# Kernel tuning notes

Measured on AMD Instinct MI355X. Metric: run time of the kernel, lower is better.

The kernel has to match this reference:

```python
import jax, jax.numpy as jnp
import numpy as np

B, L = 64, 4096
NIN, NST = 8, 16
CIN = NIN + NST          # 24 input channels to FNO
WIDTH = 64               # hidden_channels
MODES = 32               # n_modes_height
NL = 4                   # n_layers
PROJ = 128               # projection hidden width (standard FNO1d)


def setup_inputs() -> dict:
    key = jax.random.key(0)
    ks = jax.random.split(key, 12)
    u = jax.random.normal(ks[0], (B, L, NIN), jnp.float32)
    z = jax.random.normal(ks[1], (B, NST), jnp.float32)
    t = jax.random.normal(ks[2], (B,), jnp.float32)
    # lifting
    fc0_w = jax.random.normal(ks[3], (CIN, WIDTH), jnp.float32) / np.sqrt(CIN)
    fc0_b = jnp.zeros((WIDTH,), jnp.float32)
    # spectral weights (real/imag parts) and 1x1 skip convs per layer
    scale = 1.0 / (WIDTH * WIDTH)
    spec_wr = scale * jax.random.normal(ks[4], (NL, WIDTH, WIDTH, MODES), jnp.float32)
    spec_wi = scale * jax.random.normal(ks[5], (NL, WIDTH, WIDTH, MODES), jnp.float32)
    skip_w = jax.random.normal(ks[6], (NL, WIDTH, WIDTH), jnp.float32) / np.sqrt(WIDTH)
    skip_b = jnp.zeros((NL, WIDTH), jnp.float32)
    # projection
    fc1_w = jax.random.normal(ks[7], (WIDTH, PROJ), jnp.float32) / np.sqrt(WIDTH)
    fc1_b = jnp.zeros((PROJ,), jnp.float32)
    fc2_w = jax.random.normal(ks[8], (PROJ, NST), jnp.float32) / np.sqrt(PROJ)
    fc2_b = jnp.zeros((NST,), jnp.float32)
    return dict(u=u, z=z, t=t, fc0_w=fc0_w, fc0_b=fc0_b,
                spec_wr=spec_wr, spec_wi=spec_wi, skip_w=skip_w, skip_b=skip_b,
                fc1_w=fc1_w, fc1_b=fc1_b, fc2_w=fc2_w, fc2_b=fc2_b)


def _fno_forward(x, fc0_w, fc0_b, spec_wr, spec_wi, skip_w, skip_b,
                 fc1_w, fc1_b, fc2_w, fc2_b):
    # x: [B, L, CIN]
    n = x.shape[1]
    h = jnp.einsum('blc,cw->blw', x, fc0_w) + fc0_b        # lift -> [B, L, W]
    h = jnp.transpose(h, (0, 2, 1))                         # [B, W, L] channels-first
    nfreq = n // 2 + 1
    for l in range(NL):
        hf = jnp.fft.rfft(h, axis=-1)                       # [B, W, nfreq] complex
        wc = (spec_wr[l] + 1j * spec_wi[l]).astype(hf.dtype)  # [W, W, M]
        of = jnp.einsum('bim,iom->bom', hf[..., :MODES], wc)  # truncated-mode matmul
        full = jnp.zeros(h.shape[:2] + (nfreq,), hf.dtype).at[..., :MODES].set(of)
        spec = jnp.fft.irfft(full, n=n, axis=-1)            # [B, W, L]
        skip = jnp.einsum('bil,io->bol', h, skip_w[l]) + skip_b[l][None, :, None]
        h = spec + skip
        if l < NL - 1:
            h = jax.nn.gelu(h)
    h = jnp.transpose(h, (0, 2, 1))                         # [B, L, W]
    q = jax.nn.gelu(jnp.einsum('blw,wp->blp', h, fc1_w) + fc1_b)
    return jnp.einsum('blp,po->blo', q, fc2_w) + fc2_b      # [B, L, NST]


def reference(u, z, t, fc0_w, fc0_b, spec_wr, spec_wi, skip_w, skip_b,
              fc1_w, fc1_b, fc2_w, fc2_b):
    # z.tile(seq_len).reshape(B, seq_len, n_state) == broadcast along time
    rep_z = jnp.broadcast_to(z[:, None, :], (z.shape[0], u.shape[1], z.shape[1]))
    x = jnp.concatenate([u, rep_z], axis=-1)                # [B, L, CIN]
    outs = _fno_forward(x, fc0_w, fc0_b, spec_wr, spec_wi, skip_w, skip_b,
                        fc1_w, fc1_b, fc2_w, fc2_b)         # [B, L, NST]
    return outs[:, -1, :]                                   # [B, NST]
```

## Files before the change

### kernel.cpp

```cpp
#include <hip/hip_runtime.h>
#include <math.h>

#define LL 4096
#define NB 64
#define WW 64
#define NMODES 32
#define NCIN 24
#define NLAY 4
#define NPROJ 128
#define NSTC 16
#define NSPLIT 16

typedef __attribute__((ext_vector_type(8))) short short8;
typedef __attribute__((ext_vector_type(4))) float f32x4;

static __device__ __forceinline__ float gelu_fast(float x){
    const float c0 = 0.7978845608028654f;
    const float c1 = 0.044715f;
    float u = c0*(x + c1*x*x*x);
    return x / (1.0f + __expf(-2.0f*u));
}

static __device__ __forceinline__ unsigned short bf16_rn(float v){
    unsigned int u = __float_as_uint(v);
    unsigned int r = (u + 0x7fffu + ((u>>16)&1u)) >> 16;
    return (unsigned short)r;
}
static __device__ __forceinline__ float bf16f(unsigned short h){
    return __uint_as_float(((unsigned int)h)<<16);
}
static __device__ __forceinline__ void split_store(unsigned short* hi, unsigned short* lo,
                                                   size_t idx, float v){
    unsigned short h = bf16_rn(v);
    hi[idx] = h;
    lo[idx] = bf16_rn(v - bf16f(h));
}

__global__ void k_tables(unsigned short* __restrict__ TD_hi, unsigned short* __restrict__ TD_lo,
                         unsigned short* __restrict__ TIk_hi, unsigned short* __restrict__ TIk_lo){
    int idx = blockIdx.x*256 + threadIdx.x;
    if (idx >= LL*NMODES) return;
    int x = idx & (LL-1);
    int k = idx >> 12;
    int ph = (k*x) & (LL-1);
    float ang = (6.283185307179586f/(float)LL)*(float)ph;
    float c = cosf(ang), s = sinf(ang);
    split_store(TD_hi, TD_lo, (size_t)k*LL + x, c);
    split_store(TD_hi, TD_lo, (size_t)(k+NMODES)*LL + x, -s);
    float tc, ts;
    if (k == 0){ tc = 1.0f/(float)LL; ts = 0.0f; }
    else { tc = (2.0f/(float)LL)*c; ts = -(2.0f/(float)LL)*s; }
    split_store(TIk_hi, TIk_lo, (size_t)x*64 + k, tc);
    split_store(TIk_hi, TIk_lo, (size_t)x*64 + NMODES + k, ts);
}

__global__ void k_wt(const float* __restrict__ wr, const float* __restrict__ wi,
                     float* __restrict__ wrT, float* __restrict__ wiT,
                     const float* __restrict__ skw,
                     unsigned short* __restrict__ skwT_hi, unsigned short* __restrict__ skwT_lo){
    int idx = blockIdx.x*256 + threadIdx.x;
    if (idx < NLAY*WW*WW*NMODES){
        int m = idx & 31;
        int o = (idx >> 5) & 63;
        int i = (idx >> 11) & 63;
        int l = idx >> 17;
        size_t dst = (((size_t)l*NMODES + m)*WW + i)*WW + o;
        wrT[dst] = wr[idx];
        wiT[dst] = wi[idx];
    }
    if (idx < NLAY*WW*WW){
        int o = idx & 63;
        int i = (idx >> 6) & 63;
        int l = idx >> 12;
        float v = skw[((size_t)l*WW + i)*WW + o];
        split_store(skwT_hi, skwT_lo, ((size_t)l*WW + o)*WW + i, v);
    }
}

__global__ void k_lift(const float* __restrict__ u, const float* __restrict__ z,
                       const float* __restrict__ w0, const float* __restrict__ b0,
                       unsigned short* __restrict__ hT_hi, unsigned short* __restrict__ hT_lo){
    __shared__ float Ws[NCIN*WW];
    __shared__ float Bs[WW];
    __shared__ float Zs[16];
    int b = blockIdx.y;
    int x0 = blockIdx.x*256;
    int tid = threadIdx.x;
    for (int i = tid; i < NCIN*WW; i += 256) Ws[i] = w0[i];
    if (tid < WW) Bs[tid] = b0[tid];
    if (tid < 16) Zs[tid] = z[b*16 + tid];
    __syncthreads();
    int x = x0 + tid;
    const float4* up = (const float4*)(u + ((size_t)b*LL + x)*8);
    float4 a0 = up[0], a1 = up[1];
    float ur[8] = {a0.x,a0.y,a0.z,a0.w,a1.x,a1.y,a1.z,a1.w};
    float zr[16];
    #pragma unroll
    for (int j=0;j<16;j++) zr[j] = Zs[j];
    size_t rowbase = ((size_t)b*LL + x)*64;
    for (int c0=0;c0<WW;c0+=4){
        unsigned long long hv = 0ull, lv = 0ull;
        #pragma unroll
        for (int r=0;r<4;r++){
            int c = c0 + r;
            float acc = Bs[c];
            #pragma unroll
            for (int j=0;j<8;j++)  acc += ur[j]*Ws[j*WW+c];
            #pragma unroll
            for (int j=0;j<16;j++) acc += zr[j]*Ws[(8+j)*WW+c];
            unsigned short h16 = bf16_rn(acc);
            unsigned short l16 = bf16_rn(acc - bf16f(h16));
            hv |= ((unsigned long long)h16) << (16*r);
            lv |= ((unsigned long long)l16) << (16*r);
        }
        *(unsigned long long*)(hT_hi + rowbase + c0) = hv;
        *(unsigned long long*)(hT_lo + rowbase + c0) = lv;
    }
}

__global__ __launch_bounds__(256) void k_dft(
        const unsigned short* __restrict__ hT_hi, const unsigned short* __restrict__ hT_lo,
        const unsigned short* __restrict__ td_hi, const unsigned short* __restrict__ td_lo,
        float* __restrict__ part){
    int rt = blockIdx.x;
    int s  = blockIdx.y;
    int tid = threadIdx.x;
    int w = tid >> 6;
    int lane = tid & 63;
    int g = lane >> 4;
    int i = lane & 15;
    f32x4 acc[4];
    #pragma unroll
    for (int nf=0;nf<4;nf++) acc[nf] = (f32x4){0.f,0.f,0.f,0.f};
    int ch = w*16 + i;
    size_t bbase = (size_t)rt*LL;
    int xbase = s*256;
    for (int ks=0; ks<8; ks++){
        int xk = xbase + ks*32 + g*8;
        short8 a_hi, a_lo;
        size_t idx0 = (bbase + xk)*64 + ch;
        #pragma unroll
        for (int e=0;e<8;e++){
            a_hi[e] = (short)hT_hi[idx0 + (size_t)e*64];
            a_lo[e] = (short)hT_lo[idx0 + (size_t)e*64];
        }
        #pragma unroll
        for (int nf=0;nf<4;nf++){
            size_t brow = (size_t)(nf*16 + i)*LL + xk;
            short8 b_hi = *(const short8*)(td_hi + brow);
            short8 b_lo = *(const short8*)(td_lo + brow);
            acc[nf] = __builtin_amdgcn_mfma_f32_16x16x32_bf16(a_lo, b_hi, acc[nf], 0,0,0);
            acc[nf] = __builtin_amdgcn_mfma_f32_16x16x32_bf16(a_hi, b_lo, acc[nf], 0,0,0);
            acc[nf] = __builtin_amdgcn_mfma_f32_16x16x32_bf16(a_hi, b_hi, acc[nf], 0,0,0);
        }
    }
    int drow = rt*64 + w*16 + g*4;
    #pragma unroll
    for (int nf=0;nf<4;nf++)
        #pragma unroll
        for (int r=0;r<4;r++)
            part[((size_t)s*4096 + drow + r)*64 + nf*16 + i] = acc[nf][r];
}

__global__ void k_reduce(const float* __restrict__ part, float* __restrict__ hfT){
    int e = blockIdx.x*256 + threadIdx.x;
    int i    = e & 63;
    int reim = (e >> 6) & 1;
    int m    = (e >> 7) & 31;
    int b    = e >> 12;
    int n = m + 32*reim;
    size_t rowoff = ((size_t)b*WW + i)*64 + n;
    float s = 0.f;
    #pragma unroll
    for (int sp=0; sp<NSPLIT; sp++) s += part[(size_t)sp*262144 + rowoff];
    hfT[e] = s;
}

__global__ void k_mix(const float* __restrict__ hfT, const float* __restrict__ wrT,
                      const float* __restrict__ wiT, float* __restrict__ of,
                      unsigned short* __restrict__ of_hi, unsigned short* __restrict__ of_lo){
    int m = blockIdx.x, b = blockIdx.y;
    int o = threadIdx.x;
    __shared__ float hr[64], hi_[64];
    const float* row = hfT + ((size_t)b*NMODES + m)*128;
    hr[o] = row[o];
    hi_[o] = row[64+o];
    __syncthreads();
    float ar = 0.f, ai = 0.f;
    const float* wr = wrT + (size_t)m*4096;
    const float* wi = wiT + (size_t)m*4096;
    for (int i=0;i<64;i++){
        float wrv = wr[i*64+o], wiv = wi[i*64+o];
        float r = hr[i], im = hi_[i];
        ar += r*wrv - im*wiv;
        ai += r*wiv + im*wrv;
    }
    size_t base = ((size_t)b*WW+o)*64;
    of[base + m]      = ar;
    of[base + 32 + m] = ai;
    split_store(of_hi, of_lo, base + m, ar);
    split_store(of_hi, of_lo, base + 32 + m, ai);
}

__global__ __launch_bounds__(256) void k_fused(
        const unsigned short* __restrict__ hT_hi, const unsigned short* __restrict__ hT_lo,
        const unsigned short* __restrict__ tik_hi, const unsigned short* __restrict__ tik_lo,
        const unsigned short* __restrict__ skwT_hi, const unsigned short* __restrict__ skwT_lo,
        const unsigned short* __restrict__ of_hi, const unsigned short* __restrict__ of_lo,
        const float* __restrict__ skb,
        unsigned short* __restrict__ hoT_hi, unsigned short* __restrict__ hoT_lo){
    int b  = blockIdx.y;
    int X0 = blockIdx.x*64;
    int tid = threadIdx.x;
    int w = tid >> 6, lane = tid & 63, g = lane >> 4, j = lane & 15;
    int xrow = X0 + w*16 + j;
    size_t xb = ((size_t)b*LL + xrow)*64;
    size_t tb = (size_t)xrow*64;
    f32x4 acc[4];
    #pragma unroll
    for (int mf=0; mf<4; mf++) acc[mf] = (f32x4){0.f,0.f,0.f,0.f};
    #pragma unroll
    for (int ks=0; ks<4; ks++){
        int ko = ks*32 + g*8;
        const unsigned short* bp_hi = (ks < 2) ? (hT_hi + xb + ko) : (tik_hi + tb + ko - 64);
        const unsigned short* bp_lo = (ks < 2) ? (hT_lo + xb + ko) : (tik_lo + tb + ko - 64);
        short8 bh = *(const short8*)bp_hi;
        short8 bl = *(const short8*)bp_lo;
        #pragma unroll
        for (int mf=0; mf<4; mf++){
            int o = mf*16 + j;
            const unsigned short *pa_hi, *pa_lo;
            if (ks < 2){
                pa_hi = skwT_hi + (o<<6) + ko;
                pa_lo = skwT_lo + (o<<6) + ko;
            } else {
                size_t bo = ((size_t)(b*64 + o))<<6;
                pa_hi = of_hi + bo + ko - 64;
                pa_lo = of_lo + bo + ko - 64;
            }
            short8 ah = *(const short8*)pa_hi;
            short8 al = *(const short8*)pa_lo;
            acc[mf] = __builtin_amdgcn_mfma_f32_16x16x32_bf16(al, bh, acc[mf], 0,0,0);
            acc[mf] = __builtin_amdgcn_mfma_f32_16x16x32_bf16(ah, bl, acc[mf], 0,0,0);
            acc[mf] = __builtin_amdgcn_mfma_f32_16x16x32_bf16(ah, bh, acc[mf], 0,0,0);
        }
    }
    #pragma unroll
    for (int mf=0; mf<4; mf++){
        unsigned long long hv = 0ull, lv = 0ull;
        #pragma unroll
        for (int r=0; r<4; r++){
            int o = mf*16 + g*4 + r;
            float v = acc[mf][r] + skb[o];
            v = gelu_fast(v);
            unsigned short h16 = bf16_rn(v);
            unsigned short l16 = bf16_rn(v - bf16f(h16));
            hv |= ((unsigned long long)h16) << (16*r);
            lv |= ((unsigned long long)l16) << (16*r);
        }
        *(unsigned long long*)(hoT_hi + xb + mf*16 + g*4) = hv;
        *(unsigned long long*)(hoT_lo + xb + mf*16 + g*4) = lv;
    }
}

__global__ void k_final(const unsigned short* __restrict__ h3T_hi,
                        const unsigned short* __restrict__ h3T_lo,
                        const float* __restrict__ of,
                        const float* __restrict__ skw, const float* __restrict__ skb,
                        const unsigned short* __restrict__ tik_hi,
                        const unsigned short* __restrict__ tik_lo,
                        const float* __restrict__ w1, const float* __restrict__ b1,
                        const float* __restrict__ w2, const float* __restrict__ b2,
                        float* __restrict__ out){
    int b = blockIdx.x;
    int tid = threadIdx.x;
    __shared__ float hch[64];
    __shared__ float til[64];
    __shared__ float hv[64];
    __shared__ float qv[128];
    if (tid < 64){
        size_t idx = ((size_t)b*LL + (LL-1))*64 + tid;
        hch[tid] = bf16f(h3T_hi[idx]) + bf16f(h3T_lo[idx]);
    } else {
        size_t idx = (size_t)(LL-1)*64 + (tid-64);
        til[tid-64] = bf16f(tik_hi[idx]) + bf16f(tik_lo[idx]);
    }
    __syncthreads();
    if (tid < 64){
        int o = tid;
        float acc = skb[o];
        const float* ofr = of + ((size_t)b*WW + o)*64;
        #pragma unroll
        for (int j=0;j<64;j++) acc += ofr[j]*til[j];
        #pragma unroll
        for (int i=0;i<64;i++) acc += hch[i]*skw[i*64+o];
        hv[o] = acc;
    }
    __syncthreads();
    {
        int p = tid;
        float acc = b1[p];
        for (int o=0;o<64;o++) acc += hv[o]*w1[o*NPROJ+p];
        qv[p] = gelu_fast(acc);
    }
    __syncthreads();
    if (tid < NSTC){
        int s = tid;
        float acc = b2[s];
        for (int p=0;p<NPROJ;p++) acc += qv[p]*w2[p*NSTC+s];
        out[b*NSTC + s] = acc;
    }
}

extern "C" void kernel_launch(void* const* d_in, const int* in_sizes, int n_in,
                              void* d_out, int out_size, void* d_ws, size_t ws_size,
                              hipStream_t stream) {
    const float* u     = (const float*)d_in[0];
    const float* z     = (const float*)d_in[1];
    const float* fc0w  = (const float*)d_in[3];
    const float* fc0b  = (const float*)d_in[4];
    const float* swr   = (const float*)d_in[5];
    const float* swi   = (const float*)d_in[6];
    const float* skw   = (const float*)d_in[7];
    const float* skb   = (const float*)d_in[8];
    const float* fc1w  = (const float*)d_in[9];
    const float* fc1b  = (const float*)d_in[10];
    const float* fc2w  = (const float*)d_in[11];
    const float* fc2b  = (const float*)d_in[12];
    float* out = (float*)d_out;

    const size_t SZ_HP   = (size_t)NB*LL*64*2;
    const size_t SZ_TBL  = (size_t)64*LL*2;
    const size_t SZ_HFT  = (size_t)64*32*128*4;
    const size_t SZ_OF   = (size_t)64*64*64*4;
    const size_t SZ_OFP  = (size_t)64*64*64*2;
    const size_t SZ_WT   = (size_t)NLAY*NMODES*WW*WW*4;
    const size_t SZ_SKT  = (size_t)NLAY*WW*WW*2;

    size_t need = 4*SZ_HP + 4*SZ_TBL + SZ_HFT + SZ_OF + 2*SZ_OFP + 2*SZ_WT + 2*SZ_SKT;
    if (ws_size < need) return;

    char* p = (char*)d_ws;
    unsigned short* hAT_hi = (unsigned short*)p; p += SZ_HP;
    unsigned short* hAT_lo = (unsigned short*)p; p += SZ_HP;
    unsigned short* hBT_hi = (unsigned short*)p; p += SZ_HP;
    unsigned short* hBT_lo = (unsigned short*)p; p += SZ_HP;
    unsigned short* TD_hi  = (unsigned short*)p; p += SZ_TBL;
    unsigned short* TD_lo  = (unsigned short*)p; p += SZ_TBL;
    unsigned short* TIk_hi = (unsigned short*)p; p += SZ_TBL;
    unsigned short* TIk_lo = (unsigned short*)p; p += SZ_TBL;
    float* hfT   = (float*)p; p += SZ_HFT;
    float* of    = (float*)p; p += SZ_OF;
    unsigned short* of_hi = (unsigned short*)p; p += SZ_OFP;
    unsigned short* of_lo = (unsigned short*)p; p += SZ_OFP;
    float* wrT   = (float*)p; p += SZ_WT;
    float* wiT   = (float*)p; p += SZ_WT;
    unsigned short* skwT_hi = (unsigned short*)p; p += SZ_SKT;
    unsigned short* skwT_lo = (unsigned short*)p; p += SZ_SKT;

    k_tables<<<(LL*NMODES+255)/256, 256, 0, stream>>>(TD_hi, TD_lo, TIk_hi, TIk_lo);
    k_wt<<<(NLAY*WW*WW*NMODES+255)/256, 256, 0, stream>>>(swr, swi, wrT, wiT,
                                                          skw, skwT_hi, skwT_lo);
    k_lift<<<dim3(LL/256, NB), 256, 0, stream>>>(u, z, fc0w, fc0b, hAT_hi, hAT_lo);

    unsigned short* cur_hi = hAT_hi; unsigned short* cur_lo = hAT_lo;
    unsigned short* nxt_hi = hBT_hi; unsigned short* nxt_lo = hBT_lo;
    for (int l = 0; l < NLAY; l++){
        float* part = (float*)nxt_hi;
        k_dft<<<dim3(NB, NSPLIT), 256, 0, stream>>>(cur_hi, cur_lo, TD_hi, TD_lo, part);
        k_reduce<<<(64*32*128)/256, 256, 0, stream>>>(part, hfT);
        k_mix<<<dim3(NMODES, NB), 64, 0, stream>>>(hfT, wrT + (size_t)l*NMODES*WW*WW,
                                                   wiT + (size_t)l*NMODES*WW*WW,
                                                   of, of_hi, of_lo);
        if (l < NLAY-1){
            k_fused<<<dim3(LL/64, NB), 256, 0, stream>>>(cur_hi, cur_lo, TIk_hi, TIk_lo,
                skwT_hi + (size_t)l*WW*WW, skwT_lo + (size_t)l*WW*WW,
                of_hi, of_lo, skb + (size_t)l*WW, nxt_hi, nxt_lo);
            unsigned short* t;
            t = cur_hi; cur_hi = nxt_hi; nxt_hi = t;
            t = cur_lo; cur_lo = nxt_lo; nxt_lo = t;
        }
    }
    k_final<<<NB, 128, 0, stream>>>(cur_hi, cur_lo, of, skw + (size_t)3*WW*WW,
                                    skb + (size_t)3*WW, TIk_hi, TIk_lo,
                                    fc1w, fc1b, fc2w, fc2b, out);
}
```

Baseline: 720.2 us.

## Pack hi/lo bf16 pairs into 32-bit words and switch activations to channel-major layout

Activation, table and weight splits now store the bf16 hi and lo halves interleaved in one 32-bit word instead of two separate arrays. Activations become channel-major [B, C, L], so the DFT kernel reads contiguous 128-bit vectors per channel instead of strided 16-bit gathers. The fused skip/inverse kernel stages its activation and inverse-table tiles into LDS with global_load_lds and an XOR swizzle. The aim is to cut uncoalesced scalar loads in the DFT and fused kernels. The cost is repacking work in registers and scattered 32-bit output stores in the fused kernel.

```diff
diff --git a/kernel.cpp b/kernel.cpp
--- a/kernel.cpp
+++ b/kernel.cpp
@@ -14,6 +14,13 @@
 typedef __attribute__((ext_vector_type(8))) short short8;
 typedef __attribute__((ext_vector_type(4))) float f32x4;
 
+typedef const __attribute__((address_space(1))) unsigned int* gas_ptr;
+typedef __attribute__((address_space(3))) unsigned int* las_ptr;
+
+static __device__ __forceinline__ void gload16(const unsigned int* g, unsigned int* l){
+    __builtin_amdgcn_global_load_lds((gas_ptr)g, (las_ptr)l, 16, 0, 0);
+}
+
 static __device__ __forceinline__ float gelu_fast(float x){
     const float c0 = 0.7978845608028654f;
     const float c1 = 0.044715f;
@@ -29,15 +36,32 @@
 static __device__ __forceinline__ float bf16f(unsigned short h){
     return __uint_as_float(((unsigned int)h)<<16);
 }
-static __device__ __forceinline__ void split_store(unsigned short* hi, unsigned short* lo,
-                                                   size_t idx, float v){
+static __device__ __forceinline__ unsigned int pack_split(float v){
     unsigned short h = bf16_rn(v);
-    hi[idx] = h;
-    lo[idx] = bf16_rn(v - bf16f(h));
-}
-
-__global__ void k_tables(unsigned short* __restrict__ TD_hi, unsigned short* __restrict__ TD_lo,
-                         unsigned short* __restrict__ TIk_hi, unsigned short* __restrict__ TIk_lo){
+    unsigned short l = bf16_rn(v - bf16f(h));
+    return (unsigned int)h | ((unsigned int)l<<16);
+}
+static __device__ __forceinline__ float unpack_sum(unsigned int w){
+    return bf16f((unsigned short)(w & 0xffffu)) + bf16f((unsigned short)(w >> 16));
+}
+static __device__ __forceinline__ short8 hi8(uint4 a, uint4 b){
+    union { unsigned int u[4]; short8 s; } r;
+    r.u[0] = (a.x & 0xffffu) | (a.y << 16);
+    r.u[1] = (a.z & 0xffffu) | (a.w << 16);
+    r.u[2] = (b.x & 0xffffu) | (b.y << 16);
+    r.u[3] = (b.z & 0xffffu) | (b.w << 16);
+    return r.s;
+}
+static __device__ __forceinline__ short8 lo8(uint4 a, uint4 b){
+    union { unsigned int u[4]; short8 s; } r;
+    r.u[0] = (a.x >> 16) | (a.y & 0xffff0000u);
+    r.u[1] = (a.z >> 16) | (a.w & 0xffff0000u);
+    r.u[2] = (b.x >> 16) | (b.y & 0xffff0000u);
+    r.u[3] = (b.z >> 16) | (b.w & 0xffff0000u);
+    return r.s;
+}
+
+__global__ void k_tables(unsigned int* __restrict__ TD32, unsigned int* __restrict__ TI32){
     int idx = blockIdx.x*256 + threadIdx.x;
     if (idx >= LL*NMODES) return;
     int x = idx & (LL-1);
@@ -45,19 +69,18 @@
     int ph = (k*x) & (LL-1);
     float ang = (6.283185307179586f/(float)LL)*(float)ph;
     float c = cosf(ang), s = sinf(ang);
-    split_store(TD_hi, TD_lo, (size_t)k*LL + x, c);
-    split_store(TD_hi, TD_lo, (size_t)(k+NMODES)*LL + x, -s);
+    TD32[(size_t)k*LL + x]          = pack_split(c);
+    TD32[(size_t)(k+NMODES)*LL + x] = pack_split(-s);
     float tc, ts;
     if (k == 0){ tc = 1.0f/(float)LL; ts = 0.0f; }
     else { tc = (2.0f/(float)LL)*c; ts = -(2.0f/(float)LL)*s; }
-    split_store(TIk_hi, TIk_lo, (size_t)x*64 + k, tc);
-    split_store(TIk_hi, TIk_lo, (size_t)x*64 + NMODES + k, ts);
+    TI32[(size_t)k*LL + x]          = pack_split(tc);
+    TI32[(size_t)(k+NMODES)*LL + x] = pack_split(ts);
 }
 
 __global__ void k_wt(const float* __restrict__ wr, const float* __restrict__ wi,
                      float* __restrict__ wrT, float* __restrict__ wiT,
-                     const float* __restrict__ skw,
-                     unsigned short* __restrict__ skwT_hi, unsigned short* __restrict__ skwT_lo){
+                     const float* __restrict__ skw, unsigned int* __restrict__ skw32){
     int idx = blockIdx.x*256 + threadIdx.x;
     if (idx < NLAY*WW*WW*NMODES){
         int m = idx & 31;
@@ -73,13 +96,13 @@
         int i = (idx >> 6) & 63;
         int l = idx >> 12;
         float v = skw[((size_t)l*WW + i)*WW + o];
-        split_store(skwT_hi, skwT_lo, ((size_t)l*WW + o)*WW + i, v);
+        skw32[((size_t)l*WW + o)*WW + i] = pack_split(v);
     }
 }
 
 __global__ void k_lift(const float* __restrict__ u, const float* __restrict__ z,
                        const float* __restrict__ w0, const float* __restrict__ b0,
-                       unsigned short* __restrict__ hT_hi, unsigned short* __restrict__ hT_lo){
+                       unsigned int* __restrict__ h32){
     __shared__ float Ws[NCIN*WW];
     __shared__ float Bs[WW];
     __shared__ float Zs[16];
@@ -97,64 +120,54 @@
     float zr[16];
     #pragma unroll
     for (int j=0;j<16;j++) zr[j] = Zs[j];
-    size_t rowbase = ((size_t)b*LL + x)*64;
-    for (int c0=0;c0<WW;c0+=4){
-        unsigned long long hv = 0ull, lv = 0ull;
-        #pragma unroll
-        for (int r=0;r<4;r++){
-            int c = c0 + r;
-            float acc = Bs[c];
-            #pragma unroll
-            for (int j=0;j<8;j++)  acc += ur[j]*Ws[j*WW+c];
-            #pragma unroll
-            for (int j=0;j<16;j++) acc += zr[j]*Ws[(8+j)*WW+c];
-            unsigned short h16 = bf16_rn(acc);
-            unsigned short l16 = bf16_rn(acc - bf16f(h16));
-            hv |= ((unsigned long long)h16) << (16*r);
-            lv |= ((unsigned long long)l16) << (16*r);
-        }
-        *(unsigned long long*)(hT_hi + rowbase + c0) = hv;
-        *(unsigned long long*)(hT_lo + rowbase + c0) = lv;
+    for (int c=0;c<WW;c++){
+        float acc = Bs[c];
+        #pragma unroll
+        for (int j=0;j<8;j++)  acc += ur[j]*Ws[j*WW+c];
+        #pragma unroll
+        for (int j=0;j<16;j++) acc += zr[j]*Ws[(8+j)*WW+c];
+        h32[((size_t)(b*WW + c))*LL + x] = pack_split(acc);
     }
 }
 
 __global__ __launch_bounds__(256) void k_dft(
-        const unsigned short* __restrict__ hT_hi, const unsigned short* __restrict__ hT_lo,
-        const unsigned short* __restrict__ td_hi, const unsigned short* __restrict__ td_lo,
+        const unsigned int* __restrict__ h32, const unsigned int* __restrict__ td32,
         float* __restrict__ part){
-    int rt = blockIdx.x;
+    int bb = blockIdx.x;
     int s  = blockIdx.y;
     int tid = threadIdx.x;
     int w = tid >> 6;
     int lane = tid & 63;
     int g = lane >> 4;
     int i = lane & 15;
+    int ch = w*16 + i;
+    size_t abase = ((size_t)(bb*64 + ch))*LL + s*256;
+    uint4 av[16];
+    #pragma unroll
+    for (int ks=0; ks<8; ks++){
+        const uint4* ap = (const uint4*)(h32 + abase + ks*32 + g*8);
+        av[2*ks]   = ap[0];
+        av[2*ks+1] = ap[1];
+    }
     f32x4 acc[4];
     #pragma unroll
     for (int nf=0;nf<4;nf++) acc[nf] = (f32x4){0.f,0.f,0.f,0.f};
-    int ch = w*16 + i;
-    size_t bbase = (size_t)rt*LL;
-    int xbase = s*256;
+    #pragma unroll
     for (int ks=0; ks<8; ks++){
-        int xk = xbase + ks*32 + g*8;
-        short8 a_hi, a_lo;
-        size_t idx0 = (bbase + xk)*64 + ch;
-        #pragma unroll
-        for (int e=0;e<8;e++){
-            a_hi[e] = (short)hT_hi[idx0 + (size_t)e*64];
-            a_lo[e] = (short)hT_lo[idx0 + (size_t)e*64];
-        }
+        short8 ah = hi8(av[2*ks], av[2*ks+1]);
+        short8 al = lo8(av[2*ks], av[2*ks+1]);
         #pragma unroll
         for (int nf=0;nf<4;nf++){
-            size_t brow = (size_t)(nf*16 + i)*LL + xk;
-            short8 b_hi = *(const short8*)(td_hi + brow);
-            short8 b_lo = *(const short8*)(td_lo + brow);
-            acc[nf] = __builtin_amdgcn_mfma_f32_16x16x32_bf16(a_lo, b_hi, acc[nf], 0,0,0);
-            acc[nf] = __builtin_amdgcn_mfma_f32_16x16x32_bf16(a_hi, b_lo, acc[nf], 0,0,0);
-            acc[nf] = __builtin_amdgcn_mfma_f32_16x16x32_bf16(a_hi, b_hi, acc[nf], 0,0,0);
-        }
-    }
-    int drow = rt*64 + w*16 + g*4;
+            const uint4* bp = (const uint4*)(td32 + (size_t)(nf*16 + i)*LL + s*256 + ks*32 + g*8);
+            uint4 b0 = bp[0], b1 = bp[1];
+            short8 bh = hi8(b0,b1);
+            short8 bl = lo8(b0,b1);
+            acc[nf] = __builtin_amdgcn_mfma_f32_16x16x32_bf16(al, bh, acc[nf], 0,0,0);
+            acc[nf] = __builtin_amdgcn_mfma_f32_16x16x32_bf16(ah, bl, acc[nf], 0,0,0);
+            acc[nf] = __builtin_amdgcn_mfma_f32_16x16x32_bf16(ah, bh, acc[nf], 0,0,0);
+        }
+    }
+    int drow = bb*64 + w*16 + g*4;
     #pragma unroll
     for (int nf=0;nf<4;nf++)
         #pragma unroll
@@ -178,7 +191,7 @@
 
 __global__ void k_mix(const float* __restrict__ hfT, const float* __restrict__ wrT,
                       const float* __restrict__ wiT, float* __restrict__ of,
-                      unsigned short* __restrict__ of_hi, unsigned short* __restrict__ of_lo){
+                      unsigned int* __restrict__ of32){
     int m = blockIdx.x, b = blockIdx.y;
     int o = threadIdx.x;
     __shared__ float hr[64], hi_[64];
@@ -187,10 +200,10 @@
     hi_[o] = row[64+o];
     __syncthreads();
     float ar = 0.f, ai = 0.f;
-    const float* wr = wrT + (size_t)m*4096;
-    const float* wi = wiT + (size_t)m*4096;
+    const float* wrp = wrT + (size_t)m*4096;
+    const float* wip = wiT + (size_t)m*4096;
     for (int i=0;i<64;i++){
-        float wrv = wr[i*64+o], wiv = wi[i*64+o];
+        float wrv = wrp[i*64+o], wiv = wip[i*64+o];
         float r = hr[i], im = hi_[i];
         ar += r*wrv - im*wiv;
         ai += r*wiv + im*wrv;
@@ -198,48 +211,57 @@
     size_t base = ((size_t)b*WW+o)*64;
     of[base + m]      = ar;
     of[base + 32 + m] = ai;
-    split_store(of_hi, of_lo, base + m, ar);
-    split_store(of_hi, of_lo, base + 32 + m, ai);
+    of32[base + m]      = pack_split(ar);
+    of32[base + 32 + m] = pack_split(ai);
 }
 
 __global__ __launch_bounds__(256) void k_fused(
-        const unsigned short* __restrict__ hT_hi, const unsigned short* __restrict__ hT_lo,
-        const unsigned short* __restrict__ tik_hi, const unsigned short* __restrict__ tik_lo,
-        const unsigned short* __restrict__ skwT_hi, const unsigned short* __restrict__ skwT_lo,
-        const unsigned short* __restrict__ of_hi, const unsigned short* __restrict__ of_lo,
+        const unsigned int* __restrict__ h32in, const unsigned int* __restrict__ ti32,
+        const unsigned int* __restrict__ skw32, const unsigned int* __restrict__ of32,
         const float* __restrict__ skb,
-        unsigned short* __restrict__ hoT_hi, unsigned short* __restrict__ hoT_lo){
+        unsigned int* __restrict__ h32out){
+    __shared__ unsigned int tile[2*64*64];
     int b  = blockIdx.y;
     int X0 = blockIdx.x*64;
     int tid = threadIdx.x;
     int w = tid >> 6, lane = tid & 63, g = lane >> 4, j = lane & 15;
-    int xrow = X0 + w*16 + j;
-    size_t xb = ((size_t)b*LL + xrow)*64;
-    size_t tb = (size_t)xrow*64;
+    #pragma unroll
+    for (int it=0; it<4; it++){
+        int r0 = w*16 + it*4;
+        int row = r0 + (lane >> 4);
+        int p0 = (lane & 15)*4;
+        int sx = ((row >> 3) & 1) << 4;
+        gload16(h32in + ((size_t)(b*64 + row))*LL + X0 + (p0 ^ sx), &tile[r0*64]);
+        gload16(ti32  + (size_t)row*LL          + X0 + (p0 ^ sx), &tile[4096 + r0*64]);
+    }
+    __syncthreads();
     f32x4 acc[4];
     #pragma unroll
-    for (int mf=0; mf<4; mf++) acc[mf] = (f32x4){0.f,0.f,0.f,0.f};
+    for (int mf=0;mf<4;mf++) acc[mf] = (f32x4){0.f,0.f,0.f,0.f};
+    int xl = w*16 + j;
     #pragma unroll
     for (int ks=0; ks<4; ks++){
-        int ko = ks*32 + g*8;
-        const unsigned short* bp_hi = (ks < 2) ? (hT_hi + xb + ko) : (tik_hi + tb + ko - 64);
-        const unsigned short* bp_lo = (ks < 2) ? (hT_lo + xb + ko) : (tik_lo + tb + ko - 64);
-        short8 bh = *(const short8*)bp_hi;
-        short8 bl = *(const short8*)bp_lo;
+        unsigned int bv[8];
+        #pragma unroll
+        for (int e=0; e<8; e++){
+            int kr = (ks&1)*32 + g*8 + e;
+            int sx = ((kr >> 3) & 1) << 4;
+            bv[e] = tile[(ks>>1)*4096 + kr*64 + (xl ^ sx)];
+        }
+        uint4 b0 = make_uint4(bv[0],bv[1],bv[2],bv[3]);
+        uint4 b1 = make_uint4(bv[4],bv[5],bv[6],bv[7]);
+        short8 bh = hi8(b0,b1);
+        short8 bl = lo8(b0,b1);
         #pragma unroll
         for (int mf=0; mf<4; mf++){
             int o = mf*16 + j;
-            const unsigned short *pa_hi, *pa_lo;
-            if (ks < 2){
-                pa_hi = skwT_hi + (o<<6) + ko;
-                pa_lo = skwT_lo + (o<<6) + ko;
-            } else {
-                size_t bo = ((size_t)(b*64 + o))<<6;
-                pa_hi = of_hi + bo + ko - 64;
-                pa_lo = of_lo + bo + ko - 64;
-            }
-            short8 ah = *(const short8*)pa_hi;
-            short8 al = *(const short8*)pa_lo;
+            const unsigned int* pa = (ks < 2)
+                ? (skw32 + (o<<6) + ks*32 + g*8)
+                : (of32 + (((size_t)(b*64 + o))<<6) + (ks&1)*32 + g*8);
+            uint4 a0 = *(const uint4*)pa;
+            uint4 a1 = *(const uint4*)(pa + 4);
+            short8 ah = hi8(a0,a1);
+            short8 al = lo8(a0,a1);
             acc[mf] = __builtin_amdgcn_mfma_f32_16x16x32_bf16(al, bh, acc[mf], 0,0,0);
             acc[mf] = __builtin_amdgcn_mfma_f32_16x16x32_bf16(ah, bl, acc[mf], 0,0,0);
             acc[mf] = __builtin_amdgcn_mfma_f32_16x16x32_bf16(ah, bh, acc[mf], 0,0,0);
@@ -247,28 +269,19 @@
     }
     #pragma unroll
     for (int mf=0; mf<4; mf++){
-        unsigned long long hv = 0ull, lv = 0ull;
         #pragma unroll
         for (int r=0; r<4; r++){
             int o = mf*16 + g*4 + r;
             float v = acc[mf][r] + skb[o];
-            v = gelu_fast(v);
-            unsigned short h16 = bf16_rn(v);
-            unsigned short l16 = bf16_rn(v - bf16f(h16));
-            hv |= ((unsigned long long)h16) << (16*r);
-            lv |= ((unsigned long long)l16) << (16*r);
-        }
-        *(unsigned long long*)(hoT_hi + xb + mf*16 + g*4) = hv;
-        *(unsigned long long*)(hoT_lo + xb + mf*16 + g*4) = lv;
-    }
-}
-
-__global__ void k_final(const unsigned short* __restrict__ h3T_hi,
-                        const unsigned short* __restrict__ h3T_lo,
+            h32out[((size_t)(b*64 + o))*LL + X0 + xl] = pack_split(gelu_fast(v));
+        }
+    }
+}
+
+__global__ void k_final(const unsigned int* __restrict__ h32,
                         const float* __restrict__ of,
                         const float* __restrict__ skw, const float* __restrict__ skb,
-                        const unsigned short* __restrict__ tik_hi,
-                        const unsigned short* __restrict__ tik_lo,
+                        const unsigned int* __restrict__ ti32,
                         const float* __restrict__ w1, const float* __restrict__ b1,
                         const float* __restrict__ w2, const float* __restrict__ b2,
                         float* __restrict__ out){
@@ -279,11 +292,9 @@
     __shared__ float hv[64];
     __shared__ float qv[128];
     if (tid < 64){
-        size_t idx = ((size_t)b*LL + (LL-1))*64 + tid;
-        hch[tid] = bf16f(h3T_hi[idx]) + bf16f(h3T_lo[idx]);
+        hch[tid] = unpack_sum(h32[((size_t)(b*64 + tid))*LL + (LL-1)]);
     } else {
-        size_t idx = (size_t)(LL-1)*64 + (tid-64);
-        til[tid-64] = bf16f(tik_hi[idx]) + bf16f(tik_lo[idx]);
+        til[tid-64] = unpack_sum(ti32[(size_t)(tid-64)*LL + (LL-1)]);
     }
     __syncthreads();
     if (tid < 64){
@@ -329,59 +340,49 @@
     const float* fc2b  = (const float*)d_in[12];
     float* out = (float*)d_out;
 
-    const size_t SZ_HP   = (size_t)NB*LL*64*2;
-    const size_t SZ_TBL  = (size_t)64*LL*2;
+    const size_t SZ_H    = (size_t)NB*WW*LL*4;
+    const size_t SZ_TBL  = (size_t)64*LL*4;
     const size_t SZ_HFT  = (size_t)64*32*128*4;
     const size_t SZ_OF   = (size_t)64*64*64*4;
-    const size_t SZ_OFP  = (size_t)64*64*64*2;
+    const size_t SZ_OF32 = (size_t)64*64*64*4;
     const size_t SZ_WT   = (size_t)NLAY*NMODES*WW*WW*4;
-    const size_t SZ_SKT  = (size_t)NLAY*WW*WW*2;
-
-    size_t need = 4*SZ_HP + 4*SZ_TBL + SZ_HFT + SZ_OF + 2*SZ_OFP + 2*SZ_WT + 2*SZ_SKT;
+    const size_t SZ_SK32 = (size_t)NLAY*WW*WW*4;
+
+    size_t need = 2*SZ_H + 2*SZ_TBL + SZ_HFT + SZ_OF + SZ_OF32 + 2*SZ_WT + SZ_SK32;
     if (ws_size < need) return;
 
     char* p = (char*)d_ws;
-    unsigned short* hAT_hi = (unsigned short*)p; p += SZ_HP;
-    unsigned short* hAT_lo = (unsigned short*)p; p += SZ_HP;
-    unsigned short* hBT_hi = (unsigned short*)p; p += SZ_HP;
-    unsigned short* hBT_lo = (unsigned short*)p; p += SZ_HP;
-    unsigned short* TD_hi  = (unsigned short*)p; p += SZ_TBL;
-    unsigned short* TD_lo  = (unsigned short*)p; p += SZ_TBL;
-    unsigned short* TIk_hi = (unsigned short*)p; p += SZ_TBL;
-    unsigned short* TIk_lo = (unsigned short*)p; p += SZ_TBL;
+    unsigned int* hA32 = (unsigned int*)p; p += SZ_H;
+    unsigned int* hB32 = (unsigned int*)p; p += SZ_H;
+    unsigned int* TD32 = (unsigned int*)p; p += SZ_TBL;
+    unsigned int* TI32 = (unsigned int*)p; p += SZ_TBL;
     float* hfT   = (float*)p; p += SZ_HFT;
     float* of    = (float*)p; p += SZ_OF;
-    unsigned short* of_hi = (unsigned short*)p; p += SZ_OFP;
-    unsigned short* of_lo = (unsigned short*)p; p += SZ_OFP;
+    unsigned int* of32 = (unsigned int*)p; p += SZ_OF32;
     float* wrT   = (float*)p; p += SZ_WT;
     float* wiT   = (float*)p; p += SZ_WT;
-    unsigned short* skwT_hi = (unsigned short*)p; p += SZ_SKT;
-    unsigned short* skwT_lo = (unsigned short*)p; p += SZ_SKT;
-
-    k_tables<<<(LL*NMODES+255)/256, 256, 0, stream>>>(TD_hi, TD_lo, TIk_hi, TIk_lo);
-    k_wt<<<(NLAY*WW*WW*NMODES+255)/256, 256, 0, stream>>>(swr, swi, wrT, wiT,
-                                                          skw, skwT_hi, skwT_lo);
-    k_lift<<<dim3(LL/256, NB), 256, 0, stream>>>(u, z, fc0w, fc0b, hAT_hi, hAT_lo);
-
-    unsigned short* cur_hi = hAT_hi; unsigned short* cur_lo = hAT_lo;
-    unsigned short* nxt_hi = hBT_hi; unsigned short* nxt_lo = hBT_lo;
+    unsigned int* skw32 = (unsigned int*)p; p += SZ_SK32;
+
+    k_tables<<<(LL*NMODES+255)/256, 256, 0, stream>>>(TD32, TI32);
+    k_wt<<<(NLAY*WW*WW*NMODES+255)/256, 256, 0, stream>>>(swr, swi, wrT, wiT, skw, skw32);
+    k_lift<<<dim3(LL/256, NB), 256, 0, stream>>>(u, z, fc0w, fc0b, hA32);
+
+    unsigned int* cur = hA32;
+    unsigned int* nxt = hB32;
     for (int l = 0; l < NLAY; l++){
-        float* part = (float*)nxt_hi;
-        k_dft<<<dim3(NB, NSPLIT), 256, 0, stream>>>(cur_hi, cur_lo, TD_hi, TD_lo, part);
+        float* part = (float*)nxt;
+        k_dft<<<dim3(NB, NSPLIT), 256, 0, stream>>>(cur, TD32, part);
         k_reduce<<<(64*32*128)/256, 256, 0, stream>>>(part, hfT);
         k_mix<<<dim3(NMODES, NB), 64, 0, stream>>>(hfT, wrT + (size_t)l*NMODES*WW*WW,
                                                    wiT + (size_t)l*NMODES*WW*WW,
-                                                   of, of_hi, of_lo);
+                                                   of, of32);
         if (l < NLAY-1){
-            k_fused<<<dim3(LL/64, NB), 256, 0, stream>>>(cur_hi, cur_lo, TIk_hi, TIk_lo,
-                skwT_hi + (size_t)l*WW*WW, skwT_lo + (size_t)l*WW*WW,
-                of_hi, of_lo, skb + (size_t)l*WW, nxt_hi, nxt_lo);
-            unsigned short* t;
-            t = cur_hi; cur_hi = nxt_hi; nxt_hi = t;
-            t = cur_lo; cur_lo = nxt_lo; nxt_lo = t;
-        }
-    }
-    k_final<<<NB, 128, 0, stream>>>(cur_hi, cur_lo, of, skw + (size_t)3*WW*WW,
-                                    skb + (size_t)3*WW, TIk_hi, TIk_lo,
+            k_fused<<<dim3(LL/64, NB), 256, 0, stream>>>(cur, TI32,
+                skw32 + (size_t)l*WW*WW, of32, skb + (size_t)l*WW, nxt);
+            unsigned int* t = cur; cur = nxt; nxt = t;
+        }
+    }
+    k_final<<<NB, 128, 0, stream>>>(cur, of, skw + (size_t)3*WW*WW,
+                                    skb + (size_t)3*WW, TI32,
                                     fc1w, fc1b, fc2w, fc2b, out);
 }
```

After: 635.7 us. 1.13x faster.
